# Performance work log

Measured on AMD Instinct MI355X. Metric: run time of the kernel, lower is better.

Reference implementation:

```python
import jax, jax.numpy as jnp
import numpy as np

B, S, HID = 2, 1024, 2048
H, DK, DV = 8, 64, 128
TK, TV = H * DK, H * DV
K = 4                      # conv kernel size
GH = TV // 8               # generator hidden (reduction=8)
EPS = 1e-6


def setup_inputs() -> dict:
    key = jax.random.key(0)
    ks = jax.random.split(key, 10)
    sc = 0.02
    return {
        "hidden_states": jax.random.normal(ks[0], (B, S, HID), jnp.float32),
        "W_qkvabz": jax.random.normal(ks[1], (HID, TK + TK + TV + H + H + TV), jnp.float32) * sc,
        "A_log": jax.random.normal(ks[2], (H,), jnp.float32) * 0.5,
        "dt_bias": jax.random.normal(ks[3], (H,), jnp.float32) * 0.5,
        "conv_state": jax.random.normal(ks[4], (B, TV, K - 1), jnp.float32) * 0.1,
        "w1": jax.random.normal(ks[5], (HID, GH), jnp.float32) * sc,
        "w2": jax.random.normal(ks[6], (GH, TV * K), jnp.float32) * sc,
        "b2": jax.random.normal(ks[7], (TV * K,), jnp.float32) * sc,
        "init_state": jnp.zeros((B, H, DK, DV), jnp.float32),
        "o_norm_w": jnp.ones((DV,), jnp.float32),
        "W_o": jax.random.normal(ks[8], (TV, HID), jnp.float32) * sc,
    }


def _silu(x):
    return x * jax.nn.sigmoid(x)


def _l2norm(x):
    return x * jax.lax.rsqrt(jnp.sum(x * x, axis=-1, keepdims=True) + EPS)


def _dynamic_conv(v, hidden_states, conv_state, w1, w2, b2):
    # per-token depthwise conv kernels from a small MLP
    kernels = (_silu(hidden_states @ w1) @ w2 + b2).reshape(B, S, TV, K)
    # left-pad with cached state (conv_state: [B, TV, K-1] -> [B, K-1, TV])
    x_pad = jnp.concatenate([jnp.swapaxes(conv_state, 1, 2), v], axis=1)  # [B, S+K-1, TV]
    windows = jnp.stack([x_pad[:, j:j + S] for j in range(K)], axis=-1)   # [B, S, TV, K]
    return _silu(jnp.sum(windows * kernels, axis=-1))                      # [B, S, TV]


def _gated_delta_rule(q, k, v, g, beta, init_state):
    # q,k: [B,S,H,DK]; v: [B,S,H,DV]; g,beta: [B,S,H]; state: [B,H,DK,DV]
    q = _l2norm(q) * (DK ** -0.5)
    k = _l2norm(k)

    def step(h, inp):
        q_t, k_t, v_t, g_t, b_t = inp  # [B,H,DK],[B,H,DK],[B,H,DV],[B,H],[B,H]
        h = h * jnp.exp(g_t)[..., None, None]
        kv = jnp.einsum('bhk,bhkv->bhv', k_t, h)
        delta = (v_t - kv) * b_t[..., None]
        h = h + jnp.einsum('bhk,bhv->bhkv', k_t, delta)
        o_t = jnp.einsum('bhk,bhkv->bhv', q_t, h)
        return h, o_t

    xs = (jnp.moveaxis(q, 1, 0), jnp.moveaxis(k, 1, 0), jnp.moveaxis(v, 1, 0),
          jnp.moveaxis(g, 1, 0), jnp.moveaxis(beta, 1, 0))
    _, o = jax.lax.scan(step, init_state, xs)  # o: [S,B,H,DV]
    return jnp.moveaxis(o, 0, 1)               # [B,S,H,DV]


def reference(hidden_states, W_qkvabz, A_log, dt_bias, conv_state, w1, w2, b2,
              init_state, o_norm_w, W_o):
    qkvabz = hidden_states @ W_qkvabz
    q, k, v, a, beta, z = jnp.split(
        qkvabz, np.cumsum([TK, TK, TV, H, H])[:5].tolist(), axis=-1)

    q = _silu(q).reshape(B, S, H, DK)
    k = _silu(k).reshape(B, S, H, DK)

    v = _dynamic_conv(v, hidden_states, conv_state, w1, w2, b2)
    v = v.reshape(B, S, H, DV)

    g = -jnp.exp(A_log) * jax.nn.softplus(a + dt_bias)  # [B,S,H]
    beta = jax.nn.sigmoid(beta)                          # [B,S,H]

    o = _gated_delta_rule(q, k, v, g, beta, init_state)  # [B,S,H,DV]

    # gated RMSNorm: gate first, then normalize (fla GatedRMSNorm)
    z = z.reshape(B, S, H, DV)
    o = o * _silu(z)
    o = o * jax.lax.rsqrt(jnp.mean(o * o, axis=-1, keepdims=True) + EPS) * o_norm_w

    return o.reshape(B, S, TV) @ W_o
```

## Files before the change

### kernel.cpp

```cpp
#include <hip/hip_runtime.h>
#include <hip/hip_bf16.h>
#include <math.h>
#include <stdint.h>

#define BATCH 2
#define SEQ 1024
#define HIDDIM 2048
#define NH 8
#define DKD 64
#define DVD 128
#define TKD 512
#define TVD 1024
#define NCOL 3088
#define KSZ 4
#define NCHK 16

typedef __attribute__((ext_vector_type(8))) short bf16x8;
typedef __attribute__((ext_vector_type(4))) float f32x4;

__device__ __forceinline__ float sigm(float x){ return 1.f/(1.f+expf(-x)); }
__device__ __forceinline__ float siluf(float x){ return x/(1.f+expf(-x)); }
__device__ __forceinline__ float b2f(unsigned short u){
  union { unsigned int i; float f; } x; x.i = ((unsigned int)u) << 16; return x.f;
}
__device__ __forceinline__ unsigned short f2bu(float f){
  __hip_bfloat16 h = __float2bfloat16(f);
  return *(unsigned short*)&h;
}

__device__ __forceinline__ void glds16(const __hip_bfloat16* g, void* l) {
  __builtin_amdgcn_global_load_lds((const __attribute__((address_space(1))) void*)g,
                                   (__attribute__((address_space(3))) void*)l, 16, 0, 0);
}

__global__ __launch_bounds__(256) void prep_k(
    const float* __restrict__ Wqkvabz, const float* __restrict__ w1,
    const float* __restrict__ w2, const float* __restrict__ W_o,
    const float* __restrict__ hidden,
    __hip_bfloat16* __restrict__ Wcat, __hip_bfloat16* __restrict__ w2t,
    __hip_bfloat16* __restrict__ Wot, unsigned short* __restrict__ hidden_bf)
{
  __shared__ float tile[32][33];
  const int blk = blockIdx.x;
  const float* in; __hip_bfloat16* out; int R, C, bx, by;
  if (blk < 6400)      { in=Wqkvabz; out=Wcat; R=2048; C=3088; bx=blk%100; by=blk/100; }
  else if (blk < 6656) { int t=blk-6400; in=w1;  out=Wcat+(size_t)3200*2048; R=2048; C=128;  bx=t%4;   by=t/4; }
  else if (blk < 7168) { int t=blk-6656; in=w2;  out=w2t; R=128;  C=4096; bx=t%128; by=t/128; }
  else if (blk < 9216) { int t=blk-7168; in=W_o; out=Wot; R=1024; C=2048; bx=t%64;  by=t/64; }
  else {
    int i = (blk - 9216)*256 + threadIdx.x;
    float4 v = ((const float4*)hidden)[i];
    ushort4 o; o.x=f2bu(v.x); o.y=f2bu(v.y); o.z=f2bu(v.z); o.w=f2bu(v.w);
    ((ushort4*)hidden_bf)[i] = o;
    return;
  }
  const int tx = threadIdx.x & 31, ty = threadIdx.x >> 5;
  const int c = bx*32 + tx;
  #pragma unroll
  for (int i = 0; i < 4; ++i) {
    int r = by*32 + ty + i*8;
    tile[ty + i*8][tx] = (c < C) ? in[(size_t)r*C + c] : 0.f;
  }
  __syncthreads();
  #pragma unroll
  for (int i = 0; i < 4; ++i) {
    int orow = bx*32 + ty + i*8;
    int ocol = by*32 + tx;
    out[(size_t)orow*R + ocol] = __float2bfloat16(tile[tx][ty + i*8]);
  }
}

template<int EPI>
__global__ __launch_bounds__(256) void mgemm_k(
    const __hip_bfloat16* __restrict__ A,
    const __hip_bfloat16* __restrict__ Bt,
    const float* __restrict__ bias,
    float* __restrict__ Cf, __hip_bfloat16* __restrict__ Cb,
    unsigned short* __restrict__ Zb,
    int M, int N, int K, int nbx)
{
  __shared__ __hip_bfloat16 As[3][64*32];
  __shared__ __hip_bfloat16 Bs[3][128*32];
  const int tid = threadIdx.x;
  const int w = tid >> 6, l = tid & 63;
  const int wr = w >> 1, wc = w & 1;
  const int nwg = gridDim.x, q = nwg >> 3;
  const int swz = (blockIdx.x & 7)*q + (blockIdx.x >> 3);
  const int bx = swz % nbx, by = swz / nbx;
  const int row0 = by*64, col0 = bx*128;
  const int fr = l & 15, fq = l >> 4;

  f32x4 acc[2][4];
  #pragma unroll
  for (int m = 0; m < 2; ++m)
    #pragma unroll
    for (int n = 0; n < 4; ++n)
      acc[m][n] = (f32x4){0.f,0.f,0.f,0.f};

  const int ra = w*16 + (l >> 2);
  const int sg = (l & 3) ^ ((ra >> 1) & 3);
  const int ca = sg*8;

  const __hip_bfloat16* pA  = &A[(size_t)(row0 + ra)*K + ca];
  const __hip_bfloat16* pB0 = &Bt[(size_t)(col0 + ra)*K + ca];
  const __hip_bfloat16* pB1 = &Bt[(size_t)(col0 + ra + 64)*K + ca];

  glds16(pA,       (char*)&As[0][0] + w*1024);
  glds16(pB0,      (char*)&Bs[0][0] + w*1024);
  glds16(pB1,      (char*)&Bs[0][0] + 4096 + w*1024);
  if (K > 32) {
    glds16(pA  + 32, (char*)&As[1][0] + w*1024);
    glds16(pB0 + 32, (char*)&Bs[1][0] + w*1024);
    glds16(pB1 + 32, (char*)&Bs[1][0] + 4096 + w*1024);
  }
  if (K > 64) {
    glds16(pA  + 64, (char*)&As[2][0] + w*1024);
    glds16(pB0 + 64, (char*)&Bs[2][0] + w*1024);
    glds16(pB1 + 64, (char*)&Bs[2][0] + 4096 + w*1024);
  }

  int cur = 0;
  for (int k0 = 0; k0 < K; k0 += 32) {
    const int ahead = (K - k0)/32 - 1;
    if (ahead >= 2)      asm volatile("s_waitcnt vmcnt(6)" ::: "memory");
    else if (ahead == 1) asm volatile("s_waitcnt vmcnt(3)" ::: "memory");
    else                 asm volatile("s_waitcnt vmcnt(0)" ::: "memory");
    __builtin_amdgcn_s_barrier();

    bf16x8 af[2], bfv[4];
    #pragma unroll
    for (int m = 0; m < 2; ++m) {
      const int rw = wr*32 + m*16 + fr;
      af[m] = *(const bf16x8*)&As[cur][rw*32 + (fq ^ ((rw>>1)&3))*8];
    }
    #pragma unroll
    for (int n = 0; n < 4; ++n) {
      const int rw = wc*64 + n*16 + fr;
      bfv[n] = *(const bf16x8*)&Bs[cur][rw*32 + (fq ^ ((rw>>1)&3))*8];
    }
    #pragma unroll
    for (int m = 0; m < 2; ++m)
      #pragma unroll
      for (int n = 0; n < 4; ++n)
        acc[m][n] = __builtin_amdgcn_mfma_f32_16x16x32_bf16(af[m], bfv[n], acc[m][n], 0, 0, 0);

    __builtin_amdgcn_s_barrier();
    if (k0 + 96 < K) {
      glds16(pA  + k0 + 96, (char*)&As[cur][0] + w*1024);
      glds16(pB0 + k0 + 96, (char*)&Bs[cur][0] + w*1024);
      glds16(pB1 + k0 + 96, (char*)&Bs[cur][0] + 4096 + w*1024);
    }
    cur = (cur == 2) ? 0 : cur + 1;
  }

  #pragma unroll
  for (int n = 0; n < 4; ++n) {
    const int ccol = col0 + wc*64 + n*16 + fr;
    #pragma unroll
    for (int m = 0; m < 2; ++m) {
      #pragma unroll
      for (int r = 0; r < 4; ++r) {
        const int crow = row0 + wr*32 + m*16 + fq*4 + r;
        float v = acc[m][n][r];
        if (EPI == 0) {
          Cf[(size_t)crow*N + ccol] = v;
        } else if (EPI == 2) {
          Cb[(size_t)crow*N + ccol] = __float2bfloat16(v + bias[ccol]);
        } else {
          if (ccol < 2064)       Cf[(size_t)crow*NCOL + ccol] = v;
          else if (ccol < 3088)  Zb[(size_t)crow*1024 + (ccol - 2064)] = f2bu(v);
          else if (ccol >= 3200) Cb[(size_t)crow*128 + (ccol - 3200)] = __float2bfloat16(siluf(v));
        }
      }
    }
  }
}

__global__ __launch_bounds__(256) void ac_k(const float* __restrict__ qkvabz,
    const float* __restrict__ A_log, const float* __restrict__ dt_bias,
    const __hip_bfloat16* __restrict__ kern, const float* __restrict__ conv_state,
    float* __restrict__ kn, unsigned short* __restrict__ qnb,
    unsigned short* __restrict__ knb,
    float* __restrict__ g, float* __restrict__ beta, float* __restrict__ vconv)
{
  if (blockIdx.x < 4096) {
    int gid = blockIdx.x*4 + (threadIdx.x >> 6);
    int lane = threadIdx.x & 63;
    int row = gid >> 3; int h = gid & 7;
    const float* base = qkvabz + (size_t)row * NCOL;
    float qv = base[h*64 + lane];
    float kv = base[TKD + h*64 + lane];
    float sq = siluf(qv), sk = siluf(kv);
    float ssq = sq*sq, ssk = sk*sk;
    #pragma unroll
    for (int o = 32; o; o >>= 1) { ssq += __shfl_xor(ssq, o); ssk += __shfl_xor(ssk, o); }
    float qn_v = sq * rsqrtf(ssq + 1e-6f) * 0.125f;
    float kn_v = sk * rsqrtf(ssk + 1e-6f);
    size_t idx = (size_t)row*TKD + h*64 + lane;
    kn[idx]  = kn_v;
    qnb[idx] = f2bu(qn_v);
    knb[idx] = f2bu(kn_v);
    if (lane == 0) {
      float av = base[2048 + h] + dt_bias[h];
      float sp = fmaxf(av, 0.f) + log1pf(expf(-fabsf(av)));
      g[(size_t)row*NH + h] = -expf(A_log[h]) * sp;
      float bv = base[2056 + h];
      beta[(size_t)row*NH + h] = sigm(bv);
    }
  } else {
    int idx = (blockIdx.x - 4096)*256 + threadIdx.x;
    int c = idx & (TVD-1);
    int bs = idx >> 10;
    int s = bs & (SEQ-1); int b = bs >> 10;
    ushort4 kf = *(const ushort4*)&kern[(size_t)idx * 4];
    float kj[4] = { b2f(kf.x), b2f(kf.y), b2f(kf.z), b2f(kf.w) };
    float acc = 0.f;
    #pragma unroll
    for (int j = 0; j < 4; ++j) {
      int i = s + j;
      float xv = (i < 3) ? conv_state[((size_t)b*TVD + c)*3 + i]
                         : qkvabz[((size_t)(b*SEQ + (i-3)))*NCOL + TKD*2 + c];
      acc = fmaf(xv, kj[j], acc);
    }
    vconv[idx] = siluf(acc);
  }
}

__global__ __launch_bounds__(256) void chunkA_k(const float* __restrict__ kn,
   const unsigned short* __restrict__ knb,
   const float* __restrict__ vconv, const float* __restrict__ gb,
   const float* __restrict__ bb, float* __restrict__ Gcbuf,
   float* __restrict__ Dbuf, float* __restrict__ Bvec,
   unsigned short* __restrict__ UvT, unsigned short* __restrict__ WnTb)
{
  const int blk = blockIdx.x;
  const int bh = blk >> 4, c = blk & 15;
  const int b = bh >> 3, h = bh & 7;
  const int tid = threadIdx.x;
  const int w = tid >> 6, l = tid & 63;
  const int fr = l & 15, fq = l >> 4;
  const int row0 = b*SEQ + c*64;

  __shared__ unsigned short Kb[64*72];
  __shared__ float Xv[64][132];
  __shared__ float Xw[64][68];
  __shared__ float AK[64][68];
  __shared__ float Gsh[64], Bsh[64];

  #pragma unroll
  for (int j = 0; j < 2; ++j) {
    int lin = tid + j*256; int t = lin >> 3, dq = (lin & 7)*8;
    *(uint4*)&Kb[t*72+dq] = *(const uint4*)&knb[(size_t)(row0+t)*TKD + h*64 + dq];
  }
  #pragma unroll
  for (int i = 0; i < 8; ++i) {
    int lin = tid + i*256; int t = lin >> 5, v4 = (lin & 31)*4;
    float4 vv = *(const float4*)&vconv[(size_t)(row0+t)*TVD + h*128 + v4];
    Xv[t][v4]=vv.x; Xv[t][v4+1]=vv.y; Xv[t][v4+2]=vv.z; Xv[t][v4+3]=vv.w;
  }
  if (tid < 64) {
    float gv = gb[(size_t)(row0+tid)*NH + h];
    #pragma unroll
    for (int o = 1; o < 64; o <<= 1) {
      float oth = __shfl_up(gv, o);
      if (tid >= o) gv += oth;
    }
    Gsh[tid] = gv;
    Bsh[tid] = bb[(size_t)(row0+tid)*NH + h];
    Gcbuf[(size_t)blk*64 + tid] = gv;
  }
  __syncthreads();

  {
    f32x4 accS[4];
    #pragma unroll
    for (int n = 0; n < 4; ++n) accS[n] = (f32x4){0.f,0.f,0.f,0.f};
    #pragma unroll
    for (int k0 = 0; k0 < 2; ++k0) {
      bf16x8 a = *(const bf16x8*)&Kb[(w*16+fr)*72 + k0*32 + fq*8];
      #pragma unroll
      for (int n = 0; n < 4; ++n) {
        bf16x8 bb2 = *(const bf16x8*)&Kb[(n*16+fr)*72 + k0*32 + fq*8];
        accS[n] = __builtin_amdgcn_mfma_f32_16x16x32_bf16(a, bb2, accS[n], 0, 0, 0);
      }
    }
    #pragma unroll
    for (int n = 0; n < 4; ++n)
      #pragma unroll
      for (int r = 0; r < 4; ++r) {
        int t = w*16 + fq*4 + r, s = n*16 + fr;
        AK[t][s] = (s < t) ? Bsh[t]*expf(Gsh[t]-Gsh[s])*accS[n][r] : 0.f;
      }
  }
  #pragma unroll
  for (int i = 0; i < 4; ++i) {
    int lin = tid + i*256; int t = lin >> 4, d4 = (lin & 15)*4;
    float4 kv = *(const float4*)&kn[(size_t)(row0+t)*TKD + h*64 + d4];
    float f = Bsh[t]*expf(Gsh[t]);
    Xw[t][d4+0]=f*kv.x; Xw[t][d4+1]=f*kv.y; Xw[t][d4+2]=f*kv.z; Xw[t][d4+3]=f*kv.w;
  }
  __syncthreads();

  if (tid < 192) {
    float x[64];
    if (tid < 128) {
      #pragma unroll
      for (int t = 0; t < 64; ++t) x[t] = Bsh[t]*Xv[t][tid];
    } else {
      #pragma unroll
      for (int t = 0; t < 64; ++t) x[t] = Xw[t][tid-128];
    }
    #pragma unroll
    for (int t = 1; t < 64; ++t) {
      float a0=0.f, a1=0.f, a2=0.f, a3=0.f;
      #pragma unroll
      for (int s4 = 0; s4 < (t+3)/4; ++s4) {
        float4 av = *(const float4*)&AK[t][s4*4];
        a0 = fmaf(av.x, x[s4*4+0], a0);
        a1 = fmaf(av.y, x[s4*4+1], a1);
        a2 = fmaf(av.z, x[s4*4+2], a2);
        a3 = fmaf(av.w, x[s4*4+3], a3);
      }
      x[t] -= (a0+a1)+(a2+a3);
    }
    if (tid < 128) {
      #pragma unroll
      for (int t = 0; t < 64; ++t) Xv[t][tid] = x[t];
    } else {
      #pragma unroll
      for (int t = 0; t < 64; ++t) Xw[t][tid-128] = x[t];
    }
  }
  __syncthreads();

  const float Gtot = Gsh[63];
  #pragma unroll
  for (int i = 0; i < 4; ++i) {
    int lin = tid + i*256; int t = lin >> 4, d4 = (lin & 15)*4;
    float4 kv = *(const float4*)&kn[(size_t)(row0+t)*TKD + h*64 + d4];
    float f = expf(Gtot - Gsh[t]);
    AK[t][d4+0]=f*kv.x; AK[t][d4+1]=f*kv.y; AK[t][d4+2]=f*kv.z; AK[t][d4+3]=f*kv.w;
  }
  __syncthreads();

  {
    const int d1b = (tid >> 4)*4, d2b = (tid & 15)*4;
    float dacc[4][4] = {};
    #pragma unroll 8
    for (int t = 0; t < 64; ++t) {
      float4 kw = *(const float4*)&AK[t][d1b];
      float4 wv = *(const float4*)&Xw[t][d2b];
      float kwa[4] = {kw.x,kw.y,kw.z,kw.w};
      float wva[4] = {wv.x,wv.y,wv.z,wv.w};
      #pragma unroll
      for (int i = 0; i < 4; ++i)
        #pragma unroll
        for (int j = 0; j < 4; ++j)
          dacc[i][j] = fmaf(kwa[i], wva[j], dacc[i][j]);
    }
    const float eG = expf(Gtot);
    #pragma unroll
    for (int i = 0; i < 4; ++i) {
      float vals[4];
      #pragma unroll
      for (int j = 0; j < 4; ++j) {
        float v = -dacc[i][j];
        if (d1b + i == d2b + j) v += eG;
        vals[j] = v;
      }
      *(float4*)&Dbuf[(size_t)blk*4096 + (d1b+i)*64 + d2b] =
        make_float4(vals[0],vals[1],vals[2],vals[3]);
    }
  }
  {
    const int d1b = (tid >> 4)*4, vb = (tid & 15)*8;
    float bacc[4][8] = {};
    #pragma unroll 4
    for (int t = 0; t < 64; ++t) {
      float4 kw = *(const float4*)&AK[t][d1b];
      float4 u0 = *(const float4*)&Xv[t][vb];
      float4 u1 = *(const float4*)&Xv[t][vb+4];
      float kwa[4] = {kw.x,kw.y,kw.z,kw.w};
      float ua[8] = {u0.x,u0.y,u0.z,u0.w,u1.x,u1.y,u1.z,u1.w};
      #pragma unroll
      for (int i = 0; i < 4; ++i)
        #pragma unroll
        for (int j = 0; j < 8; ++j)
          bacc[i][j] = fmaf(kwa[i], ua[j], bacc[i][j]);
    }
    #pragma unroll
    for (int i = 0; i < 4; ++i) {
      *(float4*)&Bvec[(size_t)blk*8192 + (d1b+i)*128 + vb] =
        make_float4(bacc[i][0],bacc[i][1],bacc[i][2],bacc[i][3]);
      *(float4*)&Bvec[(size_t)blk*8192 + (d1b+i)*128 + vb + 4] =
        make_float4(bacc[i][4],bacc[i][5],bacc[i][6],bacc[i][7]);
    }
  }

  {
    #pragma unroll
    for (int i = 0; i < 32; ++i) {
      int v = w*32 + i;
      UvT[(size_t)blk*8192 + v*64 + l] = f2bu(Xv[l][v]);
    }
    #pragma unroll
    for (int i = 0; i < 16; ++i) {
      int d = w*16 + i;
      WnTb[(size_t)blk*4096 + d*64 + l] = f2bu(-Xw[l][d]);
    }
  }
}

__global__ __launch_bounds__(256) void chunkB2_k(const float* __restrict__ Dbuf,
   const float* __restrict__ Bvec, const float* __restrict__ init,
   unsigned short* __restrict__ HcT)
{
  const int blk = blockIdx.x;
  const int bh = blk >> 3, grp = blk & 7;
  const int v0 = grp*16;
  const int tid = threadIdx.x;
  const int v = tid & 15;
  const int d1b = (tid >> 4) * 4;
  __shared__ float DT[64][68];
  __shared__ float bsh[64][17];
  __shared__ float hsh[64][17];

  float hreg[4];
  #pragma unroll
  for (int j = 0; j < 4; ++j) {
    hreg[j] = init[((size_t)bh*64 + d1b + j)*128 + v0 + v];
    hsh[d1b + j][v] = hreg[j];
  }
  float Dreg[16], breg[4];
  {
    const float* Dp = Dbuf + (size_t)(bh*16)*4096;
    const float* bp = Bvec + (size_t)(bh*16)*8192;
    #pragma unroll
    for (int i = 0; i < 16; ++i) Dreg[i] = Dp[tid + i*256];
    #pragma unroll
    for (int i = 0; i < 4; ++i)  breg[i] = bp[(size_t)((tid>>4) + i*16)*128 + v0 + v];
  }
  #pragma unroll
  for (int i = 0; i < 16; ++i) {
    int cell = tid + i*256; DT[cell & 63][cell >> 6] = Dreg[i];
  }
  #pragma unroll
  for (int i = 0; i < 4; ++i) bsh[(tid>>4) + i*16][v] = breg[i];
  __syncthreads();

  for (int c = 0; c < 16; ++c) {
    if (c < 15) {
      const float* Dn = Dbuf + (size_t)(bh*16 + c + 1)*4096;
      const float* bn = Bvec + (size_t)(bh*16 + c + 1)*8192;
      #pragma unroll
      for (int i = 0; i < 16; ++i) Dreg[i] = Dn[tid + i*256];
      #pragma unroll
      for (int i = 0; i < 4; ++i)  breg[i] = bn[(size_t)((tid>>4) + i*16)*128 + v0 + v];
    }
    #pragma unroll
    for (int j = 0; j < 4; ++j)
      HcT[(size_t)(bh*16 + c)*8192 + (size_t)(v0+v)*64 + d1b + j] = f2bu(hreg[j]);
    float nh[4];
    #pragma unroll
    for (int j = 0; j < 4; ++j) nh[j] = bsh[d1b + j][v];
    #pragma unroll 8
    for (int d2 = 0; d2 < 64; ++d2) {
      float hv = hsh[d2][v];
      float4 dv = *(const float4*)&DT[d2][d1b];
      nh[0] = fmaf(dv.x, hv, nh[0]);
      nh[1] = fmaf(dv.y, hv, nh[1]);
      nh[2] = fmaf(dv.z, hv, nh[2]);
      nh[3] = fmaf(dv.w, hv, nh[3]);
    }
    __syncthreads();
    #pragma unroll
    for (int j = 0; j < 4; ++j) { hreg[j] = nh[j]; hsh[d1b + j][v] = nh[j]; }
    if (c < 15) {
      #pragma unroll
      for (int i = 0; i < 16; ++i) {
        int cell = tid + i*256; DT[cell & 63][cell >> 6] = Dreg[i];
      }
      #pragma unroll
      for (int i = 0; i < 4; ++i) bsh[(tid>>4) + i*16][v] = breg[i];
    }
    __syncthreads();
  }
}

__global__ __launch_bounds__(256) void chunkC_k(
   const unsigned short* __restrict__ qnb, const unsigned short* __restrict__ knb,
   const unsigned short* __restrict__ UvT, const unsigned short* __restrict__ WnTb,
   const float* __restrict__ Gcbuf, const unsigned short* __restrict__ HcT,
   const unsigned short* __restrict__ Zb, const float* __restrict__ onw,
   __hip_bfloat16* __restrict__ ofin)
{
  const int blk = blockIdx.x; const int bh = blk >> 4, c = blk & 15;
  const int b = bh >> 3, h = bh & 7;
  const int row0 = b*SEQ + c*64;
  const int tid = threadIdx.x;
  const int w = tid >> 6, l = tid & 63;
  const int fr = l & 15, fq = l >> 4;

  __shared__ unsigned short Qs[64*72];
  __shared__ unsigned short Ks[64*72];
  __shared__ unsigned short Ws[64*72];
  __shared__ unsigned short hT[128*72];
  __shared__ unsigned short UT[128*72];
  __shared__ unsigned short Ss[64*72];
  __shared__ float Gsh[64], Esh[64];

  #pragma unroll
  for (int j = 0; j < 2; ++j) {
    int lin = tid + j*256; int t = lin >> 3, dq = (lin & 7)*8;
    *(uint4*)&Qs[t*72+dq] = *(const uint4*)&qnb[(size_t)(row0+t)*TKD + h*64 + dq];
    *(uint4*)&Ks[t*72+dq] = *(const uint4*)&knb[(size_t)(row0+t)*TKD + h*64 + dq];
    *(uint4*)&Ws[t*72+dq] = *(const uint4*)&WnTb[(size_t)blk*4096 + t*64 + dq];
  }
  #pragma unroll
  for (int j = 0; j < 4; ++j) {
    int lin = tid + j*256; int v = lin >> 3, dq = (lin & 7)*8;
    *(uint4*)&hT[v*72+dq] = *(const uint4*)&HcT[(size_t)blk*8192 + (size_t)v*64 + dq];
    *(uint4*)&UT[v*72+dq] = *(const uint4*)&UvT[(size_t)blk*8192 + (size_t)v*64 + dq];
  }
  if (tid < 64) { float g = Gcbuf[(size_t)blk*64 + tid]; Gsh[tid] = g; Esh[tid] = expf(g); }
  __syncthreads();

  f32x4 accS[4];
  #pragma unroll
  for (int n = 0; n < 4; ++n) accS[n] = (f32x4){0.f,0.f,0.f,0.f};
  #pragma unroll
  for (int k0 = 0; k0 < 2; ++k0) {
    bf16x8 a = *(const bf16x8*)&Qs[(w*16+fr)*72 + k0*32 + fq*8];
    #pragma unroll
    for (int n = 0; n < 4; ++n) {
      bf16x8 bb = *(const bf16x8*)&Ks[(n*16+fr)*72 + k0*32 + fq*8];
      accS[n] = __builtin_amdgcn_mfma_f32_16x16x32_bf16(a, bb, accS[n], 0, 0, 0);
    }
  }
  #pragma unroll
  for (int n = 0; n < 4; ++n)
    #pragma unroll
    for (int r = 0; r < 4; ++r) {
      int t = w*16 + fq*4 + r, s = n*16 + fr;
      float val = (s <= t) ? expf(Gsh[t]-Gsh[s]) * accS[n][r] : 0.f;
      Ss[t*72 + s] = f2bu(val);
    }

  f32x4 accQ[4];
  #pragma unroll
  for (int n = 0; n < 4; ++n) {
    #pragma unroll
    for (int r = 0; r < 4; ++r) {
      int t = w*16 + fq*4 + r, d = n*16 + fr;
      accQ[n][r] = Esh[t] * b2f(Qs[t*72 + d]);
    }
    #pragma unroll
    for (int k0 = 0; k0 < 2; ++k0) {
      bf16x8 a = *(const bf16x8*)&Ss[(w*16+fr)*72 + k0*32 + fq*8];
      bf16x8 bb = *(const bf16x8*)&Ws[(n*16+fr)*72 + k0*32 + fq*8];
      accQ[n] = __builtin_amdgcn_mfma_f32_16x16x32_bf16(a, bb, accQ[n], 0, 0, 0);
    }
  }
  __syncthreads();

  #pragma unroll
  for (int n = 0; n < 4; ++n)
    #pragma unroll
    for (int r = 0; r < 4; ++r) {
      int t = w*16 + fq*4 + r, d = n*16 + fr;
      Ks[t*72 + d] = f2bu(accQ[n][r]);
    }

  float og[8][4];
  #pragma unroll
  for (int n = 0; n < 8; ++n) {
    f32x4 acc = (f32x4){0.f,0.f,0.f,0.f};
    #pragma unroll
    for (int k0 = 0; k0 < 2; ++k0) {
      bf16x8 a1 = *(const bf16x8*)&Ks[(w*16+fr)*72 + k0*32 + fq*8];
      bf16x8 b1 = *(const bf16x8*)&hT[(n*16+fr)*72 + k0*32 + fq*8];
      acc = __builtin_amdgcn_mfma_f32_16x16x32_bf16(a1, b1, acc, 0, 0, 0);
      bf16x8 a2 = *(const bf16x8*)&Ss[(w*16+fr)*72 + k0*32 + fq*8];
      bf16x8 b2v = *(const bf16x8*)&UT[(n*16+fr)*72 + k0*32 + fq*8];
      acc = __builtin_amdgcn_mfma_f32_16x16x32_bf16(a2, b2v, acc, 0, 0, 0);
    }
    #pragma unroll
    for (int r = 0; r < 4; ++r) og[n][r] = acc[r];
  }

  float ss0 = 0.f, ss1 = 0.f, ss2 = 0.f, ss3 = 0.f;
  #pragma unroll
  for (int n = 0; n < 8; ++n) {
    #pragma unroll
    for (int r = 0; r < 4; ++r) {
      int t = w*16 + fq*4 + r, v = n*16 + fr;
      float zf = b2f(Zb[(size_t)(row0+t)*1024 + h*128 + v]);
      float g0 = og[n][r] * siluf(zf);
      og[n][r] = g0;
      float g2 = g0*g0;
      if      (r == 0) ss0 += g2;
      else if (r == 1) ss1 += g2;
      else if (r == 2) ss2 += g2;
      else             ss3 += g2;
    }
  }
  #pragma unroll
  for (int o = 1; o <= 8; o <<= 1) {
    ss0 += __shfl_xor(ss0, o); ss1 += __shfl_xor(ss1, o);
    ss2 += __shfl_xor(ss2, o); ss3 += __shfl_xor(ss3, o);
  }
  float rr[4];
  rr[0] = rsqrtf(ss0*(1.f/128.f) + 1e-6f);
  rr[1] = rsqrtf(ss1*(1.f/128.f) + 1e-6f);
  rr[2] = rsqrtf(ss2*(1.f/128.f) + 1e-6f);
  rr[3] = rsqrtf(ss3*(1.f/128.f) + 1e-6f);
  #pragma unroll
  for (int n = 0; n < 8; ++n) {
    float ow = onw[n*16 + fr];
    #pragma unroll
    for (int r = 0; r < 4; ++r) {
      int t = w*16 + fq*4 + r, v = n*16 + fr;
      ofin[(size_t)(row0+t)*1024 + h*128 + v] = __float2bfloat16(og[n][r] * rr[r] * ow);
    }
  }
}

extern "C" void kernel_launch(void* const* d_in, const int* in_sizes, int n_in,
                              void* d_out, int out_size, void* d_ws, size_t ws_size,
                              hipStream_t stream) {
  const float* hidden     = (const float*)d_in[0];
  const float* Wqkvabz    = (const float*)d_in[1];
  const float* A_log      = (const float*)d_in[2];
  const float* dt_bias    = (const float*)d_in[3];
  const float* conv_state = (const float*)d_in[4];
  const float* w1         = (const float*)d_in[5];
  const float* w2         = (const float*)d_in[6];
  const float* b2         = (const float*)d_in[7];
  const float* init_state = (const float*)d_in[8];
  const float* o_norm_w   = (const float*)d_in[9];
  const float* W_o        = (const float*)d_in[10];
  float* out = (float*)d_out;

  float* ws = (float*)d_ws;
  float* qkvabz = ws;
  float* kern   = qkvabz + (size_t)6324224;
  float* zspare = kern   + (size_t)8388608;
  float* kn     = zspare + (size_t)1048576;
  float* gbuf   = kn     + (size_t)1048576;
  float* bbuf   = gbuf   + (size_t)16384;
  float* vconv  = bbuf   + (size_t)16384;
  float* bfpool = vconv  + (size_t)2097152;
  __hip_bfloat16* hidden_bf = (__hip_bfloat16*)bfpool;
  __hip_bfloat16* w1t   = hidden_bf + (size_t)4194304;
  __hip_bfloat16* w2t   = w1t + (size_t)262144;
  __hip_bfloat16* Wot   = w2t + (size_t)524288;
  __hip_bfloat16* x1sb  = Wot + (size_t)2097152;
  __hip_bfloat16* ofinb = x1sb + (size_t)262144;
  float* Gcbuf  = (float*)(ofinb + (size_t)2097152);
  __hip_bfloat16* Wcat   = (__hip_bfloat16*)kern;
  __hip_bfloat16* kernbf = (__hip_bfloat16*)kern;
  float* Dbuf   = kern + (size_t)2097152;
  float* Bvec   = kern + (size_t)3145728;
  unsigned short* UvTb  = (unsigned short*)(kern + (size_t)5242880);
  unsigned short* WnTbb = (unsigned short*)(kern + (size_t)6291456);
  unsigned short* qnb   = (unsigned short*)(kern + (size_t)6815744);
  unsigned short* knb   = (unsigned short*)(kern + (size_t)7340032);
  unsigned short* HcTb  = (unsigned short*)vconv;
  unsigned short* zb    = (unsigned short*)zspare;

  dim3 blk(256);
  prep_k<<<13312, blk, 0, stream>>>(Wqkvabz, w1, w2, W_o, hidden,
                                    Wcat, w2t, Wot, (unsigned short*)hidden_bf);
  mgemm_k<3><<<dim3(832),  blk, 0, stream>>>(hidden_bf, Wcat, nullptr, qkvabz, x1sb, zb, 2048, 3328, 2048, 26);
  mgemm_k<2><<<dim3(1024), blk, 0, stream>>>(x1sb, w2t, b2, nullptr, kernbf, nullptr, 2048, 4096, 128, 32);
  ac_k<<<12288, blk, 0, stream>>>(qkvabz, A_log, dt_bias, kernbf, conv_state,
                                  kn, qnb, knb, gbuf, bbuf, vconv);
  chunkA_k<<<256, blk, 0, stream>>>(kn, knb, vconv, gbuf, bbuf, Gcbuf, Dbuf, Bvec, UvTb, WnTbb);
  chunkB2_k<<<128, blk, 0, stream>>>(Dbuf, Bvec, init_state, HcTb);
  chunkC_k<<<256, blk, 0, stream>>>(qnb, knb, UvTb, WnTbb, Gcbuf, HcTb, zb, o_norm_w, ofinb);
  mgemm_k<0><<<dim3(512),  blk, 0, stream>>>(ofinb, Wot, nullptr, out, nullptr, nullptr, 2048, 2048, 1024, 16);
}
```

Measured before the change: 179.1 us.

## Enlarge GEMM tiles to 128x128 with 32x32x16 MFMA and double buffering

The shared bf16 GEMM kernel moves from 64x128 tiles using 16x16x32 MFMAs with a triple-buffered LDS pipeline to 128x128 tiles using 32x32x16 MFMAs with double buffering. The LDS swizzle, the fragment indexing and the epilogue row mapping are rewritten to match the 32x32 accumulator layout. Grid sizes are halved for all three GEMM launches. The aim is more arithmetic per loaded byte and fewer LDS reads per MFMA. In exchange there are fewer workgroups (256 for the output GEMM on a many-CU device), shallower prefetch, and more accumulator registers.

```diff
diff --git a/kernel.cpp b/kernel.cpp
--- a/kernel.cpp
+++ b/kernel.cpp
@@ -17,6 +17,7 @@
 
 typedef __attribute__((ext_vector_type(8))) short bf16x8;
 typedef __attribute__((ext_vector_type(4))) float f32x4;
+typedef __attribute__((ext_vector_type(16))) float f32x16;
 
 __device__ __forceinline__ float sigm(float x){ return 1.f/(1.f+expf(-x)); }
 __device__ __forceinline__ float siluf(float x){ return x/(1.f+expf(-x)); }
@@ -79,89 +80,89 @@
     unsigned short* __restrict__ Zb,
     int M, int N, int K, int nbx)
 {
-  __shared__ __hip_bfloat16 As[3][64*32];
-  __shared__ __hip_bfloat16 Bs[3][128*32];
+  __shared__ __hip_bfloat16 As[2][128*32];
+  __shared__ __hip_bfloat16 Bs[2][128*32];
   const int tid = threadIdx.x;
   const int w = tid >> 6, l = tid & 63;
   const int wr = w >> 1, wc = w & 1;
   const int nwg = gridDim.x, q = nwg >> 3;
   const int swz = (blockIdx.x & 7)*q + (blockIdx.x >> 3);
   const int bx = swz % nbx, by = swz / nbx;
-  const int row0 = by*64, col0 = bx*128;
-  const int fr = l & 15, fq = l >> 4;
-
-  f32x4 acc[2][4];
-  #pragma unroll
-  for (int m = 0; m < 2; ++m)
-    #pragma unroll
-    for (int n = 0; n < 4; ++n)
-      acc[m][n] = (f32x4){0.f,0.f,0.f,0.f};
+  const int row0 = by*128, col0 = bx*128;
+
+  f32x16 acc[2][2];
+  #pragma unroll
+  for (int mi = 0; mi < 2; ++mi)
+    #pragma unroll
+    for (int ni = 0; ni < 2; ++ni)
+      #pragma unroll
+      for (int r = 0; r < 16; ++r)
+        acc[mi][ni][r] = 0.f;
 
   const int ra = w*16 + (l >> 2);
-  const int sg = (l & 3) ^ ((ra >> 1) & 3);
-  const int ca = sg*8;
-
-  const __hip_bfloat16* pA  = &A[(size_t)(row0 + ra)*K + ca];
-  const __hip_bfloat16* pB0 = &Bt[(size_t)(col0 + ra)*K + ca];
-  const __hip_bfloat16* pB1 = &Bt[(size_t)(col0 + ra + 64)*K + ca];
-
-  glds16(pA,       (char*)&As[0][0] + w*1024);
+  const int sg = (l & 3) ^ ((l >> 2) & 3);
+
+  const __hip_bfloat16* pA0 = &A[(size_t)(row0 + ra)*K + sg*8];
+  const __hip_bfloat16* pA1 = &A[(size_t)(row0 + ra + 64)*K + sg*8];
+  const __hip_bfloat16* pB0 = &Bt[(size_t)(col0 + ra)*K + sg*8];
+  const __hip_bfloat16* pB1 = &Bt[(size_t)(col0 + ra + 64)*K + sg*8];
+
+  glds16(pA0,      (char*)&As[0][0] + w*1024);
+  glds16(pA1,      (char*)&As[0][0] + 4096 + w*1024);
   glds16(pB0,      (char*)&Bs[0][0] + w*1024);
   glds16(pB1,      (char*)&Bs[0][0] + 4096 + w*1024);
   if (K > 32) {
-    glds16(pA  + 32, (char*)&As[1][0] + w*1024);
+    glds16(pA0 + 32, (char*)&As[1][0] + w*1024);
+    glds16(pA1 + 32, (char*)&As[1][0] + 4096 + w*1024);
     glds16(pB0 + 32, (char*)&Bs[1][0] + w*1024);
     glds16(pB1 + 32, (char*)&Bs[1][0] + 4096 + w*1024);
   }
-  if (K > 64) {
-    glds16(pA  + 64, (char*)&As[2][0] + w*1024);
-    glds16(pB0 + 64, (char*)&Bs[2][0] + w*1024);
-    glds16(pB1 + 64, (char*)&Bs[2][0] + 4096 + w*1024);
-  }
 
   int cur = 0;
   for (int k0 = 0; k0 < K; k0 += 32) {
-    const int ahead = (K - k0)/32 - 1;
-    if (ahead >= 2)      asm volatile("s_waitcnt vmcnt(6)" ::: "memory");
-    else if (ahead == 1) asm volatile("s_waitcnt vmcnt(3)" ::: "memory");
-    else                 asm volatile("s_waitcnt vmcnt(0)" ::: "memory");
+    if (k0 + 32 < K) asm volatile("s_waitcnt vmcnt(4)" ::: "memory");
+    else             asm volatile("s_waitcnt vmcnt(0)" ::: "memory");
     __builtin_amdgcn_s_barrier();
 
-    bf16x8 af[2], bfv[4];
-    #pragma unroll
-    for (int m = 0; m < 2; ++m) {
-      const int rw = wr*32 + m*16 + fr;
-      af[m] = *(const bf16x8*)&As[cur][rw*32 + (fq ^ ((rw>>1)&3))*8];
-    }
-    #pragma unroll
-    for (int n = 0; n < 4; ++n) {
-      const int rw = wc*64 + n*16 + fr;
-      bfv[n] = *(const bf16x8*)&Bs[cur][rw*32 + (fq ^ ((rw>>1)&3))*8];
-    }
-    #pragma unroll
-    for (int m = 0; m < 2; ++m)
-      #pragma unroll
-      for (int n = 0; n < 4; ++n)
-        acc[m][n] = __builtin_amdgcn_mfma_f32_16x16x32_bf16(af[m], bfv[n], acc[m][n], 0, 0, 0);
+    #pragma unroll
+    for (int ks = 0; ks < 2; ++ks) {
+      bf16x8 af[2], bfv[2];
+      #pragma unroll
+      for (int mi = 0; mi < 2; ++mi) {
+        const int ar = wr*64 + mi*32 + (l & 31);
+        af[mi] = *(const bf16x8*)&As[cur][ar*32 + (((ks*2 + (l>>5)) ^ (ar&3)))*8];
+      }
+      #pragma unroll
+      for (int ni = 0; ni < 2; ++ni) {
+        const int br = wc*64 + ni*32 + (l & 31);
+        bfv[ni] = *(const bf16x8*)&Bs[cur][br*32 + (((ks*2 + (l>>5)) ^ (br&3)))*8];
+      }
+      #pragma unroll
+      for (int mi = 0; mi < 2; ++mi)
+        #pragma unroll
+        for (int ni = 0; ni < 2; ++ni)
+          acc[mi][ni] = __builtin_amdgcn_mfma_f32_32x32x16_bf16(af[mi], bfv[ni], acc[mi][ni], 0, 0, 0);
+    }
 
     __builtin_amdgcn_s_barrier();
-    if (k0 + 96 < K) {
-      glds16(pA  + k0 + 96, (char*)&As[cur][0] + w*1024);
-      glds16(pB0 + k0 + 96, (char*)&Bs[cur][0] + w*1024);
-      glds16(pB1 + k0 + 96, (char*)&Bs[cur][0] + 4096 + w*1024);
-    }
-    cur = (cur == 2) ? 0 : cur + 1;
-  }
-
-  #pragma unroll
-  for (int n = 0; n < 4; ++n) {
-    const int ccol = col0 + wc*64 + n*16 + fr;
-    #pragma unroll
-    for (int m = 0; m < 2; ++m) {
-      #pragma unroll
-      for (int r = 0; r < 4; ++r) {
-        const int crow = row0 + wr*32 + m*16 + fq*4 + r;
-        float v = acc[m][n][r];
+    if (k0 + 64 < K) {
+      glds16(pA0 + k0 + 64, (char*)&As[cur][0] + w*1024);
+      glds16(pA1 + k0 + 64, (char*)&As[cur][0] + 4096 + w*1024);
+      glds16(pB0 + k0 + 64, (char*)&Bs[cur][0] + w*1024);
+      glds16(pB1 + k0 + 64, (char*)&Bs[cur][0] + 4096 + w*1024);
+    }
+    cur ^= 1;
+  }
+
+  #pragma unroll
+  for (int mi = 0; mi < 2; ++mi) {
+    #pragma unroll
+    for (int ni = 0; ni < 2; ++ni) {
+      const int ccol = col0 + wc*64 + ni*32 + (l & 31);
+      #pragma unroll
+      for (int r = 0; r < 16; ++r) {
+        const int crow = row0 + wr*64 + mi*32 + (r&3) + 8*(r>>2) + 4*(l>>5);
+        float v = acc[mi][ni][r];
         if (EPI == 0) {
           Cf[(size_t)crow*N + ccol] = v;
         } else if (EPI == 2) {
@@ -671,12 +672,12 @@
   dim3 blk(256);
   prep_k<<<13312, blk, 0, stream>>>(Wqkvabz, w1, w2, W_o, hidden,
                                     Wcat, w2t, Wot, (unsigned short*)hidden_bf);
-  mgemm_k<3><<<dim3(832),  blk, 0, stream>>>(hidden_bf, Wcat, nullptr, qkvabz, x1sb, zb, 2048, 3328, 2048, 26);
-  mgemm_k<2><<<dim3(1024), blk, 0, stream>>>(x1sb, w2t, b2, nullptr, kernbf, nullptr, 2048, 4096, 128, 32);
+  mgemm_k<3><<<dim3(416),  blk, 0, stream>>>(hidden_bf, Wcat, nullptr, qkvabz, x1sb, zb, 2048, 3328, 2048, 26);
+  mgemm_k<2><<<dim3(512), blk, 0, stream>>>(x1sb, w2t, b2, nullptr, kernbf, nullptr, 2048, 4096, 128, 32);
   ac_k<<<12288, blk, 0, stream>>>(qkvabz, A_log, dt_bias, kernbf, conv_state,
                                   kn, qnb, knb, gbuf, bbuf, vconv);
   chunkA_k<<<256, blk, 0, stream>>>(kn, knb, vconv, gbuf, bbuf, Gcbuf, Dbuf, Bvec, UvTb, WnTbb);
   chunkB2_k<<<128, blk, 0, stream>>>(Dbuf, Bvec, init_state, HcTb);
   chunkC_k<<<256, blk, 0, stream>>>(qnb, knb, UvTb, WnTbb, Gcbuf, HcTb, zb, o_norm_w, ofinb);
-  mgemm_k<0><<<dim3(512),  blk, 0, stream>>>(ofinb, Wot, nullptr, out, nullptr, nullptr, 2048, 2048, 1024, 16);
-}
+  mgemm_k<0><<<dim3(256),  blk, 0, stream>>>(ofinb, Wot, nullptr, out, nullptr, nullptr, 2048, 2048, 1024, 16);
+}
```

Measured after the change: 187.3 us. 4.6% more time.
